# Kernel tuning notes

Hardware: AMD Instinct MI355X
Metric: run time of the kernel (lower is better)

The kernel has to match this reference:

```python
import jax, jax.numpy as jnp
import numpy as np

DIM = 96
HEADS = 4
HID = int(DIM * 2.66)  # 255, GDFN hidden width
B, H, W = 4, 128, 128


def _conv(x, w, b=None, groups=1):
    y = jax.lax.conv_general_dilated(x, w, (1, 1), 'SAME',
                                     dimension_numbers=('NCHW', 'OIHW', 'NCHW'),
                                     feature_group_count=groups)
    return y if b is None else y + b[None, :, None, None]


def _ln(x, w, b):
    # WithBias LayerNorm over channel dim (per pixel), biased variance, eps=1e-5
    mu = x.mean(1, keepdims=True)
    var = ((x - mu) ** 2).mean(1, keepdims=True)
    return (x - mu) / jnp.sqrt(var + 1e-5) * w[None, :, None, None] + b[None, :, None, None]


def _l2norm(x):
    # torch F.normalize(dim=-1): x / max(||x||_2, 1e-12)
    return x / jnp.maximum(jnp.linalg.norm(x, axis=-1, keepdims=True), 1e-12)


def _gelu(x):
    return jax.nn.gelu(x, approximate=False)


def setup_inputs() -> dict:
    key = jax.random.key(0)
    ks = iter(jax.random.split(key, 32))
    nrm = lambda shp, s=0.02: jax.random.normal(next(ks), shp, dtype=jnp.float32) * s
    d, h2 = DIM, HID
    inp = {
        'x': jax.random.normal(next(ks), (B, DIM, H, W), dtype=jnp.float32),
        # L_conv: 3x3(d->d,+b) GELU 1x1(d->1,+b)
        'Lc_w1': nrm((d, d, 3, 3)), 'Lc_b1': jnp.zeros((d,), jnp.float32),
        'Lc_w2': nrm((1, d, 1, 1)), 'Lc_b2': jnp.zeros((1,), jnp.float32),
        # R_conv: 3x3(d->d,+b) GELU 1x1(d->3,+b)
        'Rc_w1': nrm((d, d, 3, 3)), 'Rc_b1': jnp.zeros((d,), jnp.float32),
        'Rc_w2': nrm((3, d, 1, 1)), 'Rc_b2': jnp.zeros((3,), jnp.float32),
        # L_rein: 3x3(1->d,+b) GELU ; R_rein: 3x3(3->d,+b)
        'Lr_w': nrm((d, 1, 3, 3)), 'Lr_b': jnp.zeros((d,), jnp.float32),
        'Rr_w': nrm((d, 3, 3, 3)), 'Rr_b': jnp.zeros((d,), jnp.float32),
        # LayerNorms (WithBias)
        'n1_w': jnp.ones((d,), jnp.float32), 'n1_b': jnp.zeros((d,), jnp.float32),
        'nL_w': jnp.ones((d,), jnp.float32), 'nL_b': jnp.zeros((d,), jnp.float32),
        'n2_w': jnp.ones((d,), jnp.float32), 'n2_b': jnp.zeros((d,), jnp.float32),
        # Illum_Attention (bias=False)
        'temp': jnp.ones((HEADS, 1, 1), jnp.float32),
        'q_w': nrm((d, d, 1, 1)),
        'qd_w': nrm((d, d, 3, 3)),          # q_dwconv is a FULL 3x3 conv (no groups)
        'kv_w': nrm((2 * d, d, 1, 1)),
        'kvd_w': nrm((2 * d, 1, 3, 3)),     # depthwise, groups=2*dim
        'po_w': nrm((d, d, 1, 1)),
        # FeedForward (bias=False); NOTE: 'dwconv' here is a FULL 3x3 conv
        'pi_w': nrm((h2, d, 1, 1)),
        'fdw_w': nrm((h2, h2, 3, 3)),
        'fpo_w': nrm((d, h2, 1, 1)),
    }
    return inp


def reference(x, Lc_w1, Lc_b1, Lc_w2, Lc_b2, Rc_w1, Rc_b1, Rc_w2, Rc_b2,
              Lr_w, Lr_b, Rr_w, Rr_b, n1_w, n1_b, nL_w, nL_b, n2_w, n2_b,
              temp, q_w, qd_w, kv_w, kvd_w, po_w, pi_w, fdw_w, fpo_w):
    b, c, h, w = x.shape
    # Retinex decomposition heads
    L = _conv(_gelu(_conv(x, Lc_w1, Lc_b1)), Lc_w2, Lc_b2)   # [b,1,h,w]
    R = _conv(_gelu(_conv(x, Rc_w1, Rc_b1)), Rc_w2, Rc_b2)   # [b,3,h,w]
    L_rein = _gelu(_conv(jax.lax.stop_gradient(L), Lr_w, Lr_b))  # detach in torch
    R_rein = _conv(jax.lax.stop_gradient(R), Rr_w, Rr_b)
    # Illum_Guided_TransformerBlock: x = x + attn(norm1(x), normL(illum))
    xn = _ln(x, n1_w, n1_b)
    ill = _ln(L_rein, nL_w, nL_b)
    q = _conv(_conv(ill, q_w), qd_w)
    kv = _conv(_conv(xn, kv_w), kvd_w, groups=2 * c)
    k, v = jnp.split(kv, 2, axis=1)
    ch, hw = c // HEADS, h * w
    heads = lambda t: t.reshape(b, HEADS, ch, hw)
    qh, kh, vh = _l2norm(heads(q)), _l2norm(heads(k)), heads(v)
    # channel-wise attention: [b,heads,ch,ch]
    attn = jax.nn.softmax(jnp.einsum('bhci,bhdi->bhcd', qh, kh) * temp[None], axis=-1)
    out = jnp.einsum('bhcd,bhdi->bhci', attn, vh).reshape(b, c, h, w)
    x = x + _conv(out, po_w)
    # x = x + ffn(norm2(x))
    x2 = _ln(x, n2_w, n2_b)
    x = x + _conv(_gelu(_conv(_conv(x2, pi_w), fdw_w)), fpo_w)
    x = x + R_rein
    return (x, L, R)
```

## Files before the change

### kernel.cpp

```cpp
#include <hip/hip_runtime.h>

#define HWsz 16384
#define Wd 128

typedef unsigned short ushortT;
typedef unsigned int uintT;
typedef __attribute__((ext_vector_type(8))) short short8v;
typedef __attribute__((ext_vector_type(4))) float f32x4;
typedef __attribute__((ext_vector_type(16))) float f32x16;
typedef __attribute__((ext_vector_type(4))) unsigned short ushort4v;

__device__ __forceinline__ float gelu_f(float x){
    return 0.5f * x * (1.0f + erff(x * 0.70710678118654752f));
}
__device__ __forceinline__ ushortT f2b(float f){
    union { float f; uintT u; } v; v.f = f;
    uintT r = v.u + 0x7FFFu + ((v.u >> 16) & 1u);
    return (ushortT)(r >> 16);
}
__device__ __forceinline__ float b2f(ushortT u){
    union { uintT u; float f; } v; v.u = ((uintT)u) << 16; return v.f;
}
__device__ __forceinline__ void gload_lds16(const ushortT* g, ushortT* l){
    __builtin_amdgcn_global_load_lds(
        (const __attribute__((address_space(1))) void*)g,
        (__attribute__((address_space(3))) void*)l, 16, 0, 0);
}

__device__ __forceinline__ void pack3_one(int e, const float* __restrict__ w,
    ushortT* __restrict__ outp, int cout, int cin, int BN, int NCH)
{
    int j = e & 7; int r = e >> 3;
    int ocl = r % BN; r /= BN;
    int kg  = r & 3;  r >>= 2;
    int tap = r % 9;  r /= 9;
    int ch  = r % NCH;
    int nt  = r / NCH;
    int ci = ch*32 + kg*8 + j;
    int oc = nt*BN + ocl;
    float v = (oc < cout && ci < cin) ? w[((size_t)oc*cin + ci)*9 + tap] : 0.f;
    outp[e] = f2b(v);
}
__device__ __forceinline__ void pack1_one(int e, const float* __restrict__ w,
    ushortT* __restrict__ outp, int cout, int cin, int BN, int NCH)
{
    int j = e & 7; int r = e >> 3;
    int ocl = r % BN; r /= BN;
    int kg  = r & 3;  r >>= 2;
    int ch  = r % NCH;
    int nt  = r / NCH;
    int ci = ch*32 + kg*8 + j;
    int oc = nt*BN + ocl;
    float v = (oc < cout && ci < cin) ? w[(size_t)oc*cin + ci] : 0.f;
    outp[e] = f2b(v);
}
__global__ __launch_bounds__(256) void pack_all_kernel(
    const float* Lc, const float* Rc, const float* Qd, const float* Fd,
    const float* Q1, const float* KV1, const float* PI1, const float* FPO1,
    ushortT* dL, ushortT* dR, ushortT* dQ, ushortT* dF,
    ushortT* dq0, ushortT* dkv, ushortT* dpi, ushortT* dfpo)
{
    int e = blockIdx.x*256 + threadIdx.x;
    if      (e < 82944)  pack3_one(e,        Lc, dL, 96, 96, 48, 3);
    else if (e < 165888) pack3_one(e-82944,  Rc, dR, 96, 96, 48, 3);
    else if (e < 248832) pack3_one(e-165888, Qd, dQ, 96, 96, 32, 3);
    else if (e < 912384) pack3_one(e-248832, Fd, dF, 255,255, 48, 8);
    else if (e < 921600) pack1_one(e-912384, Q1, dq0, 96, 96, 96, 3);
    else if (e < 940032) pack1_one(e-921600, KV1,dkv, 192,96, 48, 3);
    else if (e < 964608) pack1_one(e-940032, PI1,dpi, 255,96, 64, 3);
    else if (e < 989184) pack1_one(e-964608, FPO1,dfpo,96,255, 96, 8);
}

__global__ __launch_bounds__(256) void tonhwc_ln_kernel(
    const float* __restrict__ in, const float* __restrict__ w,
    const float* __restrict__ bias, ushortT* __restrict__ xh,
    ushortT* __restrict__ xnh)
{
    const int p = blockIdx.x*256 + threadIdx.x;
    const int b = blockIdx.y;
    const float* ip = in + (size_t)b*96*HWsz + p;
    float v[96]; float s=0.f;
#pragma unroll
    for(int c=0;c<96;c++){ v[c]=ip[(size_t)c*HWsz]; s+=v[c]; }
    const float mu = s*(1.f/96.f);
    float s2=0.f;
#pragma unroll
    for(int c=0;c<96;c++){ float d=v[c]-mu; s2+=d*d; }
    const float inv = 1.f/sqrtf(s2*(1.f/96.f)+1e-5f);
    ushortT* op1 = xh  + ((size_t)b*HWsz + p)*96;
    ushortT* op2 = xnh + ((size_t)b*HWsz + p)*96;
#pragma unroll
    for (int g=0; g<12; g++){
        uint4 pk1, pk2; uintT a4[4], n4[4];
#pragma unroll
        for (int i=0;i<4;i++){
            float x0 = v[g*8+2*i], x1v = v[g*8+2*i+1];
            a4[i] = (uintT)f2b(x0) | ((uintT)f2b(x1v)<<16);
            float r0 = (x0-mu)*inv*w[g*8+2*i]+bias[g*8+2*i];
            float r1 = (x1v-mu)*inv*w[g*8+2*i+1]+bias[g*8+2*i+1];
            n4[i] = (uintT)f2b(r0) | ((uintT)f2b(r1)<<16);
        }
        pk1.x=a4[0]; pk1.y=a4[1]; pk1.z=a4[2]; pk1.w=a4[3];
        pk2.x=n4[0]; pk2.y=n4[1]; pk2.z=n4[2]; pk2.w=n4[3];
        *(uint4*)(op1 + g*8) = pk1;
        *(uint4*)(op2 + g*8) = pk2;
    }
}

template<int NG, int NCH, int ACT, int TWOOUT>
__global__ __launch_bounds__(256,3) void conv3x3_v4(
    const ushortT* __restrict__ inh,
    const ushortT* __restrict__ wpk1, const ushortT* __restrict__ wpk2,
    const float* __restrict__ bias1, const float* __restrict__ bias2,
    ushortT* __restrict__ out1, ushortT* __restrict__ out2,
    int cout, int ocpad)
{
    constexpr int BN = NG*16;
    constexpr int Cpad = NCH*32;
    constexpr int WCH4 = 9*4*BN;
    constexpr int WI = (WCH4 + 255)/256;
    __shared__ __align__(16) ushortT As[4*324*8];
    __shared__ __align__(16) ushortT Ws[WCH4*8];

    const int tid = threadIdx.x;
    const int l   = tid & 63;
    const int wv  = tid >> 6;
    const int l15 = l & 15;
    const int kg  = l >> 4;
    const int tix = blockIdx.x & 7, tiy = blockIdx.x >> 3;
    const int b   = blockIdx.z;
    const int x0 = tix*16, y0 = tiy*16;

    int nt = blockIdx.y;
    const ushortT* wpk; const float* bias; ushortT* outp; int ntw;
    if (TWOOUT && nt >= 2){ wpk = wpk2; bias = bias2; outp = out2; ntw = nt-2; }
    else { wpk = wpk1; bias = bias1; outp = out1; ntw = nt; }
    const int ocbase = ntw*BN;

    f32x4 acc[4][NG];
#pragma unroll
    for (int m=0;m<4;m++)
#pragma unroll
        for (int n=0;n<NG;n++) acc[m][n] = (f32x4){0.f,0.f,0.f,0.f};

    const ushortT* inb = inh + (size_t)b*HWsz*Cpad;

    for (int ch=0; ch<NCH; ch++){
        __syncthreads();
        for (int t=tid; t<1296; t+=256){
            int p = t>>2, g = t&3;
            int hy = p/18, hx = p - hy*18;
            int gy = y0 + hy - 1, gx = x0 + hx - 1;
            uint4 v; v.x=0u; v.y=0u; v.z=0u; v.w=0u;
            if ((unsigned)gy < 128u && (unsigned)gx < 128u)
                v = *(const uint4*)(inb + (size_t)(gy*Wd+gx)*Cpad + ch*32 + g*8);
            *(uint4*)(As + (g*324+p)*8) = v;
        }
        {
            const ushortT* wsrc = wpk + ((size_t)ntw*NCH + ch)*(WCH4*8);
#pragma unroll
            for (int i=0; i<WI; i++){
                int t = i*256 + tid;
                if ((WCH4 & 255) == 0 || t < WCH4)
                    gload_lds16(wsrc + (size_t)t*8, Ws + (size_t)t*8);
            }
        }
        __syncthreads();
#pragma unroll
        for (int tp=0; tp<9; tp++){
            const int dy = tp/3, dx = tp - dy*3;
            short8v bf[NG];
#pragma unroll
            for (int n=0;n<NG;n++)
                bf[n] = *(const short8v*)(Ws + ((size_t)(tp*4 + kg)*BN + n*16 + l15)*8);
#pragma unroll
            for (int mg=0;mg<4;mg++){
                short8v a = *(const short8v*)(As + (kg*324 + (wv*4+mg+dy)*18 + l15+dx)*8);
#pragma unroll
                for (int n=0;n<NG;n++)
                    acc[mg][n] = __builtin_amdgcn_mfma_f32_16x16x32_bf16(a, bf[n], acc[mg][n], 0,0,0);
            }
        }
    }
    __syncthreads();
    ushortT* Ts = As + wv*1024;
#pragma unroll
    for (int mg=0;mg<4;mg++){
        int gy = y0 + wv*4 + mg;
        ushortT* orow = outp + ((size_t)b*HWsz + gy*Wd + x0)*ocpad + ocbase;
#pragma unroll
        for (int n=0;n<NG;n++){
            int ocl = n*16 + l15;
            int oc  = ocbase + ocl;
            float bs = (bias && oc < cout) ? bias[oc] : 0.f;
#pragma unroll
            for (int j=0;j<4;j++){
                int pxj = kg*4 + j;
                float r = 0.f;
                if (oc < cout){ r = acc[mg][n][j] + bs; if (ACT) r = gelu_f(r); }
                int seg = ((ocl>>3) + pxj) & 7;
                Ts[pxj*64 + seg*8 + (ocl&7)] = f2b(r);
            }
        }
#pragma unroll
        for (int ps=0; ps < (BN+31)/32; ps++){
            int rpx = l & 15;
            int rs  = (l>>4) + ps*4;
            if (rs*8 < BN){
                int pseg = (rs + rpx) & 7;
                short8v v = *(const short8v*)(Ts + rpx*64 + pseg*8);
                *(short8v*)(orow + (size_t)rpx*ocpad + rs*8) = v;
            }
        }
    }
}

template<int NGW, int NCH>
__global__ __launch_bounds__(256) void gemm1x1_v2(
    const ushortT* __restrict__ inh, const ushortT* __restrict__ wpk,
    ushortT* __restrict__ outp, int cout, int ocpad)
{
    constexpr int BN = NGW*16;
    constexpr int Cpad = NCH*32;
    __shared__ __align__(16) ushortT Ts[4*16*64];

    const int tid = threadIdx.x;
    const int l = tid & 63, wv = tid >> 6, l15 = l & 15, kg = l >> 4;
    const int p0 = blockIdx.x*64;
    const int b  = blockIdx.z;
    const int nt = wv, ocbase = wv*BN;
    const ushortT* inb = inh + (size_t)b*HWsz*Cpad;

    f32x4 acc[4][NGW];
#pragma unroll
    for (int m=0;m<4;m++)
#pragma unroll
        for (int n=0;n<NGW;n++) acc[m][n] = (f32x4){0.f,0.f,0.f,0.f};

#pragma unroll
    for (int ch=0; ch<NCH; ch++){
        short8v a[4], bw[NGW];
#pragma unroll
        for (int mg=0; mg<4; mg++)
            a[mg] = *(const short8v*)(inb + (size_t)(p0 + mg*16 + l15)*Cpad + ch*32 + kg*8);
#pragma unroll
        for (int n=0;n<NGW;n++)
            bw[n] = *(const short8v*)(wpk + (((size_t)(nt*NCH + ch)*4 + kg)*BN + n*16 + l15)*8);
#pragma unroll
        for (int mg=0;mg<4;mg++)
#pragma unroll
            for (int n=0;n<NGW;n++)
                acc[mg][n] = __builtin_amdgcn_mfma_f32_16x16x32_bf16(a[mg], bw[n], acc[mg][n], 0,0,0);
    }
    ushortT* Tw = Ts + wv*1024;
#pragma unroll
    for (int mg=0;mg<4;mg++){
        ushortT* orow = outp + ((size_t)b*HWsz + p0 + mg*16)*ocpad + ocbase;
#pragma unroll
        for (int n=0;n<NGW;n++){
            int ocl = n*16 + l15;
            int oc  = ocbase + ocl;
#pragma unroll
            for (int j=0;j<4;j++){
                int pxj = kg*4 + j;
                float r = (oc < cout) ? acc[mg][n][j] : 0.f;
                int seg = ((ocl>>3) + pxj) & 7;
                Tw[pxj*64 + seg*8 + (ocl&7)] = f2b(r);
            }
        }
#pragma unroll
        for (int ps=0; ps < (BN+31)/32; ps++){
            int rpx = l & 15;
            int rs  = (l>>4) + ps*4;
            if (rs*8 < BN){
                int pseg = (rs + rpx) & 7;
                short8v v = *(const short8v*)(Tw + rpx*64 + pseg*8);
                *(short8v*)(orow + (size_t)rpx*ocpad + rs*8) = v;
            }
        }
    }
}

template<int NG, int NCH, int ACT, int OMODE, int NSPLIT, int XMAP>
__global__ __launch_bounds__(256,4) void conv3x3_mfma(
    const ushortT* __restrict__ inh,
    const ushortT* __restrict__ wpk1, const ushortT* __restrict__ wpk2,
    const float* __restrict__ bias1, const float* __restrict__ bias2,
    void* __restrict__ out1, void* __restrict__ out2,
    int cout, int ocpad)
{
    constexpr int BN = NG*16;
    constexpr int Cpad = NCH*32;
    __shared__ __align__(16) ushortT As[4*324*8];

    const int tid = threadIdx.x;
    const int l   = tid & 63;
    const int wv  = tid >> 6;
    const int l15 = l & 15;
    const int kg  = l >> 4;
    int tile = blockIdx.x, nt = blockIdx.y, b = blockIdx.z;
    const int tix = tile & 7, tiy = tile >> 3;

    const ushortT* wpk = wpk1; const float* bias = bias1; void* outv = out1;
    if (NSPLIT > 0 && nt >= NSPLIT){ nt -= NSPLIT; wpk = wpk2; bias = bias2; outv = out2; }

    f32x4 acc[4][NG];
#pragma unroll
    for (int m=0;m<4;m++)
#pragma unroll
        for (int n=0;n<NG;n++) acc[m][n] = (f32x4){0.f,0.f,0.f,0.f};

    const ushortT* inb = inh + (size_t)b*HWsz*Cpad;

    for (int ch=0; ch<NCH; ch++){
        __syncthreads();
#pragma unroll
        for (int g=0; g<4; g++){
            for (int p=tid; p<324; p+=256){
                int hy = p/18, hx = p - hy*18;
                int gy = tiy*16 + hy - 1, gx = tix*16 + hx - 1;
                uint4 v; v.x=0u; v.y=0u; v.z=0u; v.w=0u;
                if ((unsigned)gy < 128u && (unsigned)gx < 128u)
                    v = *(const uint4*)(inb + (size_t)(gy*Wd+gx)*Cpad + ch*32 + g*8);
                *(uint4*)(As + (g*324+p)*8) = v;
            }
        }
        __syncthreads();
        const ushortT* wch = wpk + (size_t)(nt*NCH + ch)*(9*4*BN*8);
#pragma unroll
        for (int tp=0; tp<9; tp++){
            const int dy = tp/3, dx = tp - dy*3;
            short8v a[4], bf[NG];
#pragma unroll
            for (int mg=0; mg<4; mg++){
                int p = (wv*4 + mg + dy)*18 + l15 + dx;
                a[mg] = *(const short8v*)(As + (kg*324 + p)*8);
            }
#pragma unroll
            for (int n=0;n<NG;n++)
                bf[n] = *(const short8v*)(wch + ((size_t)(tp*4 + kg)*BN + n*16 + l15)*8);
#pragma unroll
            for (int mg=0;mg<4;mg++)
#pragma unroll
                for (int n=0;n<NG;n++)
                    acc[mg][n] = __builtin_amdgcn_mfma_f32_16x16x32_bf16(a[mg], bf[n], acc[mg][n], 0,0,0);
        }
    }
    if (OMODE == 2){
        ushortT* out = (ushortT*)outv;
#pragma unroll
        for (int n=0;n<NG;n++){
            int oc = nt*BN + n*16 + l15;
            if (oc < cout){
                float bs = bias ? bias[oc] : 0.f;
#pragma unroll
                for (int mg=0;mg<4;mg++){
                    int gy = tiy*16 + wv*4 + mg;
                    int gx = tix*16 + kg*4;
                    ushort4v pk;
#pragma unroll
                    for (int j=0;j<4;j++){
                        float r = acc[mg][n][j] + bs;
                        if (ACT) r = gelu_f(r);
                        pk[j] = f2b(r);
                    }
                    *(ushort4v*)(out + ((size_t)b*cout + oc)*HWsz + gy*Wd + gx) = pk;
                }
            }
        }
    }
}

template<int NG, int NCH, int RES, int OMODE, int XMAP>
__global__ __launch_bounds__(256) void gemm1x1_mfma(
    const ushortT* __restrict__ inh, const ushortT* __restrict__ wpk, int wstride_z,
    const float* __restrict__ res1, const ushortT* __restrict__ res2b,
    void* __restrict__ outv, int cout, int ocpad)
{
    constexpr int BN = NG*16;
    constexpr int Cpad = NCH*32;
    constexpr int LSTR = (BN <= 64) ? 64 : 128;
    constexpr int MASK = LSTR/8 - 1;
    __shared__ __align__(16) ushortT TsS[(OMODE==1) ? 4*16*LSTR : 16];

    const int tid = threadIdx.x;
    const int l = tid & 63, wv = tid >> 6, l15 = l & 15, kg = l >> 4;
    int chunk = blockIdx.x, nt = blockIdx.y, b = blockIdx.z;
    const int p0 = chunk*256 + wv*64;
    const ushortT* inb = inh + (size_t)b*HWsz*Cpad;
    const ushortT* wp  = wpk + (size_t)b*wstride_z;

    f32x4 acc[4][NG];
#pragma unroll
    for (int m=0;m<4;m++)
#pragma unroll
        for (int n=0;n<NG;n++) acc[m][n] = (f32x4){0.f,0.f,0.f,0.f};

#pragma unroll
    for (int ch=0; ch<NCH; ch++){
        short8v a[4], bw[NG];
#pragma unroll
        for (int mg=0; mg<4; mg++)
            a[mg] = *(const short8v*)(inb + (size_t)(p0 + mg*16 + l15)*Cpad + ch*32 + kg*8);
#pragma unroll
        for (int n=0;n<NG;n++)
            bw[n] = *(const short8v*)(wp + (((size_t)(nt*NCH + ch)*4 + kg)*BN + n*16 + l15)*8);
#pragma unroll
        for (int mg=0;mg<4;mg++)
#pragma unroll
            for (int n=0;n<NG;n++)
                acc[mg][n] = __builtin_amdgcn_mfma_f32_16x16x32_bf16(a[mg], bw[n], acc[mg][n], 0,0,0);
    }
    if (OMODE == 0){
        float* out = (float*)outv;
#pragma unroll
        for (int n=0;n<NG;n++){
            int oc = nt*BN + n*16 + l15;
            if (oc < cout){
#pragma unroll
                for (int mg=0;mg<4;mg++){
                    int pix = p0 + mg*16 + kg*4;
                    size_t idx = ((size_t)b*cout + oc)*HWsz + pix;
                    float4 r;
                    r.x = acc[mg][n][0]; r.y = acc[mg][n][1];
                    r.z = acc[mg][n][2]; r.w = acc[mg][n][3];
                    if (RES>=1){ float4 q = *(const float4*)(res1+idx); r.x+=q.x;r.y+=q.y;r.z+=q.z;r.w+=q.w; }
                    if (RES>=2){
                        ushort4v q = *(const ushort4v*)(res2b+idx);
                        r.x+=b2f(q[0]); r.y+=b2f(q[1]); r.z+=b2f(q[2]); r.w+=b2f(q[3]);
                    }
                    *(float4*)(out + idx) = r;
                }
            }
        }
    } else {
        ushortT* outp = (ushortT*)outv;
        ushortT* Ts = TsS + wv*(16*LSTR);
#pragma unroll
        for (int mg=0;mg<4;mg++){
            ushortT* orow = outp + ((size_t)b*HWsz + p0 + mg*16)*ocpad + nt*BN;
#pragma unroll
            for (int n=0;n<NG;n++){
                int ocl = n*16 + l15;
                int oc  = nt*BN + ocl;
#pragma unroll
                for (int j=0;j<4;j++){
                    int pxj = kg*4 + j;
                    float r = (oc < cout) ? acc[mg][n][j] : 0.f;
                    int seg = ((ocl>>3) + pxj) & MASK;
                    Ts[pxj*LSTR + seg*8 + (ocl&7)] = f2b(r);
                }
            }
#pragma unroll
            for (int ps=0; ps < (BN+31)/32; ps++){
                int rpx = l & 15;
                int rs  = (l>>4) + ps*4;
                if (rs*8 < BN){
                    int pseg = (rs + rpx) & MASK;
                    short8v v = *(const short8v*)(Ts + rpx*LSTR + pseg*8);
                    *(short8v*)(orow + (size_t)rpx*ocpad + rs*8) = v;
                }
            }
        }
    }
}

__global__ __launch_bounds__(256) void pvpo_ln_kernel(
    const ushortT* __restrict__ vh, const ushortT* __restrict__ Mpk,
    const float* __restrict__ xres, const float* __restrict__ lnw,
    const float* __restrict__ lnb, float* __restrict__ x1out,
    ushortT* __restrict__ x2nh)
{
    constexpr int BN = 96, NG = 6, NCH = 3, Cpad = 96, LSTR = 128, MASK = 15;
    __shared__ __align__(16) ushortT TsS[4*16*LSTR];

    const int tid = threadIdx.x;
    const int l = tid & 63, wv = tid >> 6, l15 = l & 15, kg = l >> 4;
    const int b = blockIdx.z;
    const int p0 = blockIdx.x*256 + wv*64;
    const ushortT* inb = vh + (size_t)b*HWsz*Cpad;
    const ushortT* wp  = Mpk + (size_t)b*9216;

    f32x4 acc[4][NG];
#pragma unroll
    for (int m=0;m<4;m++)
#pragma unroll
        for (int n=0;n<NG;n++) acc[m][n] = (f32x4){0.f,0.f,0.f,0.f};

#pragma unroll
    for (int ch=0; ch<NCH; ch++){
        short8v a[4], bw[NG];
#pragma unroll
        for (int mg=0; mg<4; mg++)
            a[mg] = *(const short8v*)(inb + (size_t)(p0 + mg*16 + l15)*Cpad + ch*32 + kg*8);
#pragma unroll
        for (int n=0;n<NG;n++)
            bw[n] = *(const short8v*)(wp + (((size_t)ch*4 + kg)*BN + n*16 + l15)*8);
#pragma unroll
        for (int mg=0;mg<4;mg++)
#pragma unroll
            for (int n=0;n<NG;n++)
                acc[mg][n] = __builtin_amdgcn_mfma_f32_16x16x32_bf16(a[mg], bw[n], acc[mg][n], 0,0,0);
    }
    float mu_[4], inv_[4];
#pragma unroll
    for (int mg=0;mg<4;mg++){
#pragma unroll
        for (int n=0;n<NG;n++){
            int oc = n*16 + l15;
            int pix = p0 + mg*16 + kg*4;
            size_t idx = ((size_t)b*96 + oc)*HWsz + pix;
            float4 q = *(const float4*)(xres+idx);
            acc[mg][n][0] += q.x; acc[mg][n][1] += q.y;
            acc[mg][n][2] += q.z; acc[mg][n][3] += q.w;
            float4 r;
            r.x = acc[mg][n][0]; r.y = acc[mg][n][1];
            r.z = acc[mg][n][2]; r.w = acc[mg][n][3];
            *(float4*)(x1out + idx) = r;
        }
    }
    float nv[4][NG][4];
#pragma unroll
    for (int mg=0;mg<4;mg++){
#pragma unroll
        for (int j=0;j<4;j++){
            float s = 0.f, s2 = 0.f;
#pragma unroll
            for (int n=0;n<NG;n++){ float v = acc[mg][n][j]; s += v; s2 += v*v; }
#pragma unroll
            for (int m=1; m<16; m<<=1){
                s  += __shfl_xor(s, m, 64);
                s2 += __shfl_xor(s2, m, 64);
            }
            float mu = s*(1.f/96.f);
            float var = s2*(1.f/96.f) - mu*mu;
            float inv = 1.f/sqrtf(var + 1e-5f);
#pragma unroll
            for (int n=0;n<NG;n++){
                int oc = n*16 + l15;
                nv[mg][n][j] = (acc[mg][n][j]-mu)*inv*lnw[oc]+lnb[oc];
            }
        }
    }
    ushortT* Ts = TsS + wv*(16*LSTR);
#pragma unroll
    for (int mg=0;mg<4;mg++){
        ushortT* orow = x2nh + ((size_t)b*HWsz + p0 + mg*16)*96;
#pragma unroll
        for (int n=0;n<NG;n++){
            int ocl = n*16 + l15;
#pragma unroll
            for (int j=0;j<4;j++){
                int pxj = kg*4 + j;
                int seg = ((ocl>>3) + pxj) & MASK;
                Ts[pxj*LSTR + seg*8 + (ocl&7)] = f2b(nv[mg][n][j]);
            }
        }
#pragma unroll
        for (int ps=0; ps<3; ps++){
            int rpx = l & 15;
            int rs  = (l>>4) + ps*4;
            int pseg = (rs + rpx) & MASK;
            short8v v = *(const short8v*)(Ts + rpx*LSTR + pseg*8);
            *(short8v*)(orow + (size_t)rpx*96 + rs*8) = v;
        }
    }
}

template<int NOUT>
__global__ __launch_bounds__(256) void head1x1_kernel(
    const ushortT* __restrict__ inh, const float* __restrict__ w,
    const float* __restrict__ bias, float* __restrict__ out)
{
    __shared__ float lw[NOUT*96];
    const int tid = threadIdx.x;
    for (int t=tid; t<NOUT*96; t+=256) lw[t] = w[t];
    __syncthreads();
    const int p = blockIdx.x*256 + tid;
    const int b = blockIdx.y;
    const ushortT* ip = inh + ((size_t)b*HWsz + p)*96;
    float v[96];
#pragma unroll
    for (int g=0; g<12; g++){
        short8v s = *(const short8v*)(ip + g*8);
#pragma unroll
        for (int i=0;i<8;i++) v[g*8+i] = b2f((ushortT)s[i]);
    }
#pragma unroll
    for (int oc=0; oc<NOUT; oc++){
        float acc = bias[oc];
#pragma unroll
        for (int c=0;c<96;c++) acc += v[c]*lw[oc*96+c];
        out[((size_t)b*NOUT + oc)*HWsz + p] = acc;
    }
}

__global__ __launch_bounds__(256) void lrein_ln_kernel(
    const float* __restrict__ L, const float* __restrict__ w,
    const float* __restrict__ bias, const float* __restrict__ lnw,
    const float* __restrict__ lnb, ushortT* __restrict__ outh)
{
    __shared__ float sw[864], sb[96], sn1[96], sn2[96];
    const int tid = threadIdx.x;
    for (int t=tid; t<864; t+=256) sw[t] = w[t];
    if (tid < 96){ sb[tid]=bias[tid]; sn1[tid]=lnw[tid]; sn2[tid]=lnb[tid]; }
    __syncthreads();
    const int p = blockIdx.x*256 + tid;
    const int b = blockIdx.y;
    const int y = p>>7, x = p&127;
    const float* ib = L + (size_t)b*HWsz;
    float win[9];
#pragma unroll
    for (int dy=0;dy<3;dy++)
#pragma unroll
        for (int dx=0;dx<3;dx++){
            int gy=y+dy-1, gx=x+dx-1;
            win[dy*3+dx] = ((unsigned)gy<128u && (unsigned)gx<128u) ? ib[gy*Wd+gx] : 0.f;
        }
    float v[96]; float s=0.f;
#pragma unroll
    for (int c=0;c<96;c++){
        float a = sb[c];
#pragma unroll
        for (int t=0;t<9;t++) a += win[t]*sw[c*9+t];
        a = gelu_f(a);
        v[c]=a; s+=a;
    }
    const float mu = s*(1.f/96.f);
    float s2=0.f;
#pragma unroll
    for (int c=0;c<96;c++){ float d=v[c]-mu; s2+=d*d; }
    const float inv = 1.f/sqrtf(s2*(1.f/96.f)+1e-5f);
    ushortT* op = outh + ((size_t)b*HWsz + p)*96;
#pragma unroll
    for (int g=0; g<12; g++){
        uint4 pk; uintT w4[4];
#pragma unroll
        for (int i=0;i<4;i++){
            float r0 = (v[g*8+2*i]-mu)*inv*sn1[g*8+2*i]+sn2[g*8+2*i];
            float r1 = (v[g*8+2*i+1]-mu)*inv*sn1[g*8+2*i+1]+sn2[g*8+2*i+1];
            w4[i] = (uintT)f2b(r0) | ((uintT)f2b(r1)<<16);
        }
        pk.x=w4[0]; pk.y=w4[1]; pk.z=w4[2]; pk.w=w4[3];
        *(uint4*)(op + g*8) = pk;
    }
}

__global__ __launch_bounds__(256) void conv3x3_rr_kernel(
    const float* __restrict__ in, const float* __restrict__ w,
    const float* __restrict__ bias, ushortT* __restrict__ out)
{
    __shared__ float sw[216], sb[8];
    const int oc0 = blockIdx.y*8;
    if (threadIdx.x < 216) sw[threadIdx.x] = w[(size_t)oc0*27 + threadIdx.x];
    if (threadIdx.x < 8)   sb[threadIdx.x] = bias[oc0 + threadIdx.x];
    __syncthreads();
    const int p = blockIdx.x*256+threadIdx.x;
    const int b = blockIdx.z;
    const int y=p>>7, x=p&127;
    const float* ib = in + (size_t)b*3*HWsz;
    float win[27];
#pragma unroll
    for (int ci=0;ci<3;ci++)
#pragma unroll
        for (int dy=0;dy<3;dy++)
#pragma unroll
            for (int dx=0;dx<3;dx++){
                int gy=y+dy-1, gx=x+dx-1;
                win[ci*9+dy*3+dx] = ((unsigned)gy<128u && (unsigned)gx<128u)
                    ? ib[(size_t)ci*HWsz + gy*Wd+gx] : 0.f;
            }
#pragma unroll
    for (int i=0;i<8;i++){
        float acc = sb[i];
#pragma unroll
        for (int t=0;t<27;t++) acc += win[t]*sw[i*27+t];
        out[((size_t)b*96 + oc0+i)*HWsz + p] = f2b(acc);
    }
}

__global__ __launch_bounds__(256) void dw_nhwc_kernel(
    const ushortT* __restrict__ inh, const float* __restrict__ w,
    ushortT* __restrict__ kout, ushortT* __restrict__ vouth)
{
    const int p = blockIdx.x*256+threadIdx.x;
    const int c0 = blockIdx.y*8;
    const int b = blockIdx.z;
    const int y=p>>7, x=p&127;
    float lw[72];
#pragma unroll
    for (int i=0;i<8;i++)
#pragma unroll
        for (int t=0;t<9;t++) lw[i*9+t] = w[(size_t)(c0+i)*9 + t];
    const ushortT* ib = inh + (size_t)b*HWsz*192;
    float acc[8];
#pragma unroll
    for (int i=0;i<8;i++) acc[i]=0.f;
#pragma unroll
    for(int dy=0;dy<3;dy++){
        int gy=y+dy-1;
        if((unsigned)gy<128u){
#pragma unroll
            for(int dx=0;dx<3;dx++){
                int gx=x+dx-1;
                if((unsigned)gx<128u){
                    short8v s = *(const short8v*)(ib + (size_t)(gy*Wd+gx)*192 + c0);
#pragma unroll
                    for (int i=0;i<8;i++) acc[i] += b2f((ushortT)s[i])*lw[i*9+dy*3+dx];
                }
            }
        }
    }
    if (c0 < 96){
#pragma unroll
        for (int i=0;i<8;i++)
            kout[((size_t)b*96 + c0+i)*HWsz + p] = f2b(acc[i]);
    } else {
        ushortT* op = vouth + ((size_t)b*HWsz + p)*96 + (c0-96);
        uint4 pk;
        pk.x = (uintT)f2b(acc[0]) | ((uintT)f2b(acc[1])<<16);
        pk.y = (uintT)f2b(acc[2]) | ((uintT)f2b(acc[3])<<16);
        pk.z = (uintT)f2b(acc[4]) | ((uintT)f2b(acc[5])<<16);
        pk.w = (uintT)f2b(acc[6]) | ((uintT)f2b(acc[7])<<16);
        *(uint4*)op = pk;
    }
}

__global__ __launch_bounds__(256) void rownorm_bf16_kernel(
    const ushortT* __restrict__ qb, const ushortT* __restrict__ kb,
    float* __restrict__ invqk)
{
    __shared__ float red[256];
    const int r = blockIdx.x;
    const ushortT* ip = (r < 384) ? (qb + (size_t)r*HWsz) : (kb + (size_t)(r-384)*HWsz);
    float s=0.f;
    const ushortT* tp = ip + threadIdx.x*64;
#pragma unroll
    for (int g=0; g<8; g++){
        short8v v = *(const short8v*)(tp + g*8);
#pragma unroll
        for (int i=0;i<8;i++){ float f = b2f((ushortT)v[i]); s += f*f; }
    }
    red[threadIdx.x]=s; __syncthreads();
    for(int st=128; st>0; st>>=1){
        if(threadIdx.x<st) red[threadIdx.x]+=red[threadIdx.x+st];
        __syncthreads();
    }
    if(threadIdx.x==0) invqk[r] = 1.f/fmaxf(sqrtf(red[0]), 1e-12f);
}

__global__ __launch_bounds__(256) void qk_mfma_kernel(
    const ushortT* __restrict__ qb, const ushortT* __restrict__ kb,
    float* __restrict__ part)
{
    const int tid = threadIdx.x;
    const int l = tid & 63, wv = tid >> 6;
    const int chunk = blockIdx.x*4 + wv;
    const int bh = blockIdx.y, b = bh>>2, h = bh&3;
    const int ch = min(l & 31, 23);
    const int kh = (l >> 5)*8;
    const ushortT* qp = qb + ((size_t)b*96 + h*24 + ch)*HWsz + chunk*512 + kh;
    const ushortT* kp = kb + ((size_t)b*96 + h*24 + ch)*HWsz + chunk*512 + kh;
    f32x16 acc;
#pragma unroll
    for (int r=0;r<16;r++) acc[r]=0.f;
    for (int ks=0; ks<32; ks++){
        short8v a  = *(const short8v*)(qp + ks*16);
        short8v bb = *(const short8v*)(kp + ks*16);
        acc = __builtin_amdgcn_mfma_f32_32x32x16_bf16(a, bb, acc, 0,0,0);
    }
    float* op = part + ((size_t)chunk*16 + bh)*1024;
    const int col = l & 31;
#pragma unroll
    for (int r=0;r<16;r++){
        int row = (r&3) + 8*(r>>2) + 4*(l>>5);
        op[row*32 + col] = acc[r];
    }
}

__global__ void qk_reduce_kernel(const float* __restrict__ part, float* __restrict__ out)
{
    int idx = blockIdx.x*256+threadIdx.x;
    float s=0.f;
    for(int c=0;c<32;c++) s += part[(size_t)c*16384 + idx];
    out[idx]=s;
}

__global__ __launch_bounds__(576) void softmax_kernel(
    const float* __restrict__ raw, const float* __restrict__ invq,
    const float* __restrict__ invk, const float* __restrict__ temp,
    float* __restrict__ attn)
{
    __shared__ float l[576];
    const int bh=blockIdx.x, b=bh>>2, h=bh&3;
    const int tid=threadIdx.x;
    const int i=tid/24, j=tid-i*24;
    l[tid] = raw[(size_t)bh*1024 + i*32 + j] * invq[b*96+h*24+i] * invk[b*96+h*24+j] * temp[h];
    __syncthreads();
    if(tid<24){
        float m=-1e30f;
#pragma unroll
        for(int jj=0;jj<24;jj++) m = fmaxf(m, l[tid*24+jj]);
        float e[24]; float s=0.f;
#pragma unroll
        for(int jj=0;jj<24;jj++){ e[jj]=__expf(l[tid*24+jj]-m); s+=e[jj]; }
        float isv = 1.f/s;
#pragma unroll
        for(int jj=0;jj<24;jj++) attn[(size_t)bh*576 + tid*24 + jj] = e[jj]*isv;
    }
}

__global__ __launch_bounds__(256) void mkM_kernel(
    const float* __restrict__ attn, const float* __restrict__ po_w,
    ushortT* __restrict__ Mpk)
{
    const int b = blockIdx.x;
    for (int e = threadIdx.x; e < 9216; e += 256){
        int oc = e / 96, d = e - oc*96;
        int h = d / 24, dl = d - h*24;
        const float* aw = attn + ((size_t)(b*4+h))*576 + dl;
        const float* pw = po_w + (size_t)oc*96 + h*24;
        float s = 0.f;
#pragma unroll
        for (int c=0;c<24;c++) s += pw[c]*aw[c*24];
        int ch = d>>5, kg = (d>>3)&3, j = d&7;
        Mpk[(size_t)b*9216 + ((size_t)(ch*4+kg)*96 + oc)*8 + j] = f2b(s);
    }
}

extern "C" void kernel_launch(void* const* d_in, const int* in_sizes, int n_in,
                              void* d_out, int out_size, void* d_ws, size_t ws_size,
                              hipStream_t stream)
{
    const float* x     = (const float*)d_in[0];
    const float* Lc_w1 = (const float*)d_in[1];
    const float* Lc_b1 = (const float*)d_in[2];
    const float* Lc_w2 = (const float*)d_in[3];
    const float* Lc_b2 = (const float*)d_in[4];
    const float* Rc_w1 = (const float*)d_in[5];
    const float* Rc_b1 = (const float*)d_in[6];
    const float* Rc_w2 = (const float*)d_in[7];
    const float* Rc_b2 = (const float*)d_in[8];
    const float* Lr_w  = (const float*)d_in[9];
    const float* Lr_b  = (const float*)d_in[10];
    const float* Rr_w  = (const float*)d_in[11];
    const float* Rr_b  = (const float*)d_in[12];
    const float* n1_w  = (const float*)d_in[13];
    const float* n1_b  = (const float*)d_in[14];
    const float* nL_w  = (const float*)d_in[15];
    const float* nL_b  = (const float*)d_in[16];
    const float* n2_w  = (const float*)d_in[17];
    const float* n2_b  = (const float*)d_in[18];
    const float* temp  = (const float*)d_in[19];
    const float* q_w   = (const float*)d_in[20];
    const float* qd_w  = (const float*)d_in[21];
    const float* kv_w  = (const float*)d_in[22];
    const float* kvd_w = (const float*)d_in[23];
    const float* po_w  = (const float*)d_in[24];
    const float* pi_w  = (const float*)d_in[25];
    const float* fdw_w = (const float*)d_in[26];
    const float* fpo_w = (const float*)d_in[27];

    char* base = (char*)d_ws;
    ushortT* xh   = (ushortT*)(base + 0);
    ushortT* f0h  = (ushortT*)(base + 0);
    ushortT* Lh   = (ushortT*)(base + 33554432);
    ushortT* kv0h = (ushortT*)(base + 33554432);
    ushortT* f1h  = (ushortT*)(base + 33554432);
    ushortT* Rh   = (ushortT*)(base + 67108864);
    ushortT* vh   = (ushortT*)(base + 67108864);
    ushortT* x2nh = (ushortT*)(base + 67108864);
    ushortT* illh = (ushortT*)(base + 79691776);
    ushortT* xnh  = (ushortT*)(base + 92274688);
    ushortT* q0h  = (ushortT*)(base + 104857600);
    ushortT* qb   = (ushortT*)(base + 117440512);
    float*   x1   = (float*)(base + 117440512);
    ushortT* kb   = (ushortT*)(base + 142606336);
    ushortT* Bb   = (ushortT*)(base + 155189248);
    char* smb = base + 167772160;
    ushortT* wpkL = (ushortT*)smb;   smb += 165888;
    ushortT* wpkR = (ushortT*)smb;   smb += 165888;
    ushortT* wpkQ = (ushortT*)smb;   smb += 165888;
    ushortT* wpkF = (ushortT*)smb;   smb += 1327104;
    ushortT* wq0  = (ushortT*)smb;   smb += 18432;
    ushortT* wkv  = (ushortT*)smb;   smb += 36864;
    ushortT* wpi  = (ushortT*)smb;   smb += 49152;
    ushortT* wfpo = (ushortT*)smb;   smb += 49152;
    ushortT* Mpk  = (ushortT*)smb;   smb += 73728;
    float* invqk  = (float*)smb;     smb += 3072;
    float* part   = (float*)smb;     smb += 2097152;
    float* araw   = (float*)smb;     smb += 65536;
    float* attn   = (float*)smb;     smb += 36864;

    float* out_x = (float*)d_out;
    float* out_L = out_x + (size_t)4*96*HWsz;
    float* out_R = out_L + (size_t)4*HWsz;

    dim3 blk(256);

    hipLaunchKernelGGL(pack_all_kernel, dim3(3864), blk, 0, stream,
        Lc_w1, Rc_w1, qd_w, fdw_w, q_w, kv_w, pi_w, fpo_w,
        wpkL, wpkR, wpkQ, wpkF, wq0, wkv, wpi, wfpo);
    hipLaunchKernelGGL(tonhwc_ln_kernel, dim3(64,4), blk, 0, stream, x, n1_w, n1_b, xh, xnh);

    hipLaunchKernelGGL((conv3x3_v4<3,3,1,1>), dim3(64,4,4), blk, 0, stream,
        xh, wpkL, wpkR, Lc_b1, Rc_b1, Lh, Rh, 96, 96);
    hipLaunchKernelGGL((head1x1_kernel<1>), dim3(64,4), blk, 0, stream, Lh, Lc_w2, Lc_b2, out_L);
    hipLaunchKernelGGL((head1x1_kernel<3>), dim3(64,4), blk, 0, stream, Rh, Rc_w2, Rc_b2, out_R);
    hipLaunchKernelGGL(lrein_ln_kernel, dim3(64,4), blk, 0, stream, out_L, Lr_w, Lr_b, nL_w, nL_b, illh);
    hipLaunchKernelGGL(conv3x3_rr_kernel, dim3(64,12,4), blk, 0, stream, out_R, Rr_w, Rr_b, Bb);

    hipLaunchKernelGGL((gemm1x1_mfma<6,3,0,1,0>), dim3(64,1,4), blk, 0, stream,
        illh, wq0, 0, nullptr, nullptr, (void*)q0h, 96, 96);
    hipLaunchKernelGGL((conv3x3_mfma<2,3,0,2,0,0>), dim3(64,3,4), blk, 0, stream,
        q0h, wpkQ, wpkQ, nullptr, nullptr, (void*)qb, (void*)qb, 96, 0);
    hipLaunchKernelGGL((gemm1x1_v2<3,3>), dim3(256,1,4), blk, 0, stream,
        xnh, wkv, kv0h, 192, 192);
    hipLaunchKernelGGL(dw_nhwc_kernel, dim3(64,24,4), blk, 0, stream, kv0h, kvd_w, kb, vh);

    hipLaunchKernelGGL(rownorm_bf16_kernel, dim3(768), blk, 0, stream, qb, kb, invqk);
    hipLaunchKernelGGL(qk_mfma_kernel, dim3(8,16), blk, 0, stream, qb, kb, part);
    hipLaunchKernelGGL(qk_reduce_kernel, dim3(64), blk, 0, stream, part, araw);
    hipLaunchKernelGGL(softmax_kernel, dim3(16), dim3(576), 0, stream, araw, invqk, invqk+384, temp, attn);
    hipLaunchKernelGGL(mkM_kernel, dim3(4), blk, 0, stream, attn, po_w, Mpk);
    hipLaunchKernelGGL(pvpo_ln_kernel, dim3(64,1,4), blk, 0, stream,
        vh, Mpk, x, n2_w, n2_b, x1, x2nh);

    hipLaunchKernelGGL((gemm1x1_v2<4,3>), dim3(256,1,4), blk, 0, stream,
        x2nh, wpi, f0h, 255, 256);
    hipLaunchKernelGGL((conv3x3_v4<3,8,1,0>), dim3(64,6,4), blk, 0, stream,
        f0h, wpkF, wpkF, nullptr, nullptr, f1h, f1h, 255, 256);
    hipLaunchKernelGGL((gemm1x1_mfma<6,8,2,0,0>), dim3(64,1,4), blk, 0, stream,
        f1h, wfpo, 0, x1, Bb, (void*)out_x, 96, 0);
}
```

Before: 373.6 us.

## Add two-batch 3x3 conv tiles, reuse v4 conv for q, fuse qk reduce into softmax

Adds conv3x3_tt, which processes two batch images per block so each weight chunk loaded into LDS is reused across both images. The Lc/Rc and FFN depthwise-replacement 3x3 convs now use it, with half as many blocks. The q 3x3 conv switches to conv3x3_v4 with a new planar output mode and a 48-wide N tile. The qk partial reduction is folded into the softmax kernel, and LN variance becomes two-pass. Changes touch occupancy (launch bounds 2, doubled LDS) and remove one launch.

```diff
diff --git a/kernel.cpp b/kernel.cpp
--- a/kernel.cpp
+++ b/kernel.cpp
@@ -63,7 +63,7 @@
     int e = blockIdx.x*256 + threadIdx.x;
     if      (e < 82944)  pack3_one(e,        Lc, dL, 96, 96, 48, 3);
     else if (e < 165888) pack3_one(e-82944,  Rc, dR, 96, 96, 48, 3);
-    else if (e < 248832) pack3_one(e-165888, Qd, dQ, 96, 96, 32, 3);
+    else if (e < 248832) pack3_one(e-165888, Qd, dQ, 96, 96, 48, 3);
     else if (e < 912384) pack3_one(e-248832, Fd, dF, 255,255, 48, 8);
     else if (e < 921600) pack1_one(e-912384, Q1, dq0, 96, 96, 96, 3);
     else if (e < 940032) pack1_one(e-921600, KV1,dkv, 192,96, 48, 3);
@@ -108,6 +108,125 @@
 }
 
 template<int NG, int NCH, int ACT, int TWOOUT>
+__global__ __launch_bounds__(256,2) void conv3x3_tt(
+    const ushortT* __restrict__ inh,
+    const ushortT* __restrict__ wpk1, const ushortT* __restrict__ wpk2,
+    const float* __restrict__ bias1, const float* __restrict__ bias2,
+    ushortT* __restrict__ out1, ushortT* __restrict__ out2,
+    int cout, int ocpad)
+{
+    constexpr int BN = NG*16;
+    constexpr int Cpad = NCH*32;
+    constexpr int WCH4 = 9*4*BN;
+    constexpr int WI = (WCH4 + 255)/256;
+    __shared__ __align__(16) ushortT As[2*4*324*8];
+    __shared__ __align__(16) ushortT Ws[WCH4*8];
+
+    const int tid = threadIdx.x;
+    const int l   = tid & 63;
+    const int wv  = tid >> 6;
+    const int l15 = l & 15;
+    const int kg  = l >> 4;
+    const int tix = blockIdx.x & 7, tiy = blockIdx.x >> 3;
+    const int b0  = blockIdx.z*2;
+    const int x0 = tix*16, y0 = tiy*16;
+
+    int nt = blockIdx.y;
+    const ushortT* wpk; const float* bias; ushortT* outp; int ntw;
+    if (TWOOUT && nt >= 2){ wpk = wpk2; bias = bias2; outp = out2; ntw = nt-2; }
+    else { wpk = wpk1; bias = bias1; outp = out1; ntw = nt; }
+    const int ocbase = ntw*BN;
+
+    f32x4 acc[2][4][NG];
+#pragma unroll
+    for (int tl=0;tl<2;tl++)
+#pragma unroll
+        for (int m=0;m<4;m++)
+#pragma unroll
+            for (int n=0;n<NG;n++) acc[tl][m][n] = (f32x4){0.f,0.f,0.f,0.f};
+
+    for (int ch=0; ch<NCH; ch++){
+        __syncthreads();
+#pragma unroll
+        for (int tl=0; tl<2; tl++){
+            const ushortT* inb = inh + (size_t)(b0+tl)*HWsz*Cpad;
+            for (int t=tid; t<1296; t+=256){
+                int p = t>>2, g = t&3;
+                int hy = p/18, hx = p - hy*18;
+                int gy = y0 + hy - 1, gx = x0 + hx - 1;
+                uint4 v; v.x=0u; v.y=0u; v.z=0u; v.w=0u;
+                if ((unsigned)gy < 128u && (unsigned)gx < 128u)
+                    v = *(const uint4*)(inb + (size_t)(gy*Wd+gx)*Cpad + ch*32 + g*8);
+                *(uint4*)(As + (tl*1296 + g*324 + p)*8) = v;
+            }
+        }
+        {
+            const ushortT* wsrc = wpk + ((size_t)ntw*NCH + ch)*(WCH4*8);
+#pragma unroll
+            for (int i=0; i<WI; i++){
+                int t = i*256 + tid;
+                if ((WCH4 & 255) == 0 || t < WCH4)
+                    gload_lds16(wsrc + (size_t)t*8, Ws + (size_t)t*8);
+            }
+        }
+        __syncthreads();
+#pragma unroll
+        for (int tp=0; tp<9; tp++){
+            const int dy = tp/3, dx = tp - dy*3;
+            short8v bf[NG];
+#pragma unroll
+            for (int n=0;n<NG;n++)
+                bf[n] = *(const short8v*)(Ws + ((size_t)(tp*4 + kg)*BN + n*16 + l15)*8);
+#pragma unroll
+            for (int tl=0;tl<2;tl++){
+#pragma unroll
+                for (int mg=0;mg<4;mg++){
+                    short8v a = *(const short8v*)(As + (tl*1296 + kg*324 + (wv*4+mg+dy)*18 + l15+dx)*8);
+#pragma unroll
+                    for (int n=0;n<NG;n++)
+                        acc[tl][mg][n] = __builtin_amdgcn_mfma_f32_16x16x32_bf16(a, bf[n], acc[tl][mg][n], 0,0,0);
+                }
+            }
+        }
+    }
+    __syncthreads();
+    ushortT* Ts = As + wv*1024;
+#pragma unroll
+    for (int tl=0;tl<2;tl++){
+        ushortT* outb = outp + (size_t)(b0+tl)*HWsz*ocpad;
+#pragma unroll
+        for (int mg=0;mg<4;mg++){
+            int gy = y0 + wv*4 + mg;
+            ushortT* orow = outb + ((size_t)gy*Wd + x0)*ocpad + ocbase;
+#pragma unroll
+            for (int n=0;n<NG;n++){
+                int ocl = n*16 + l15;
+                int oc  = ocbase + ocl;
+                float bs = (bias && oc < cout) ? bias[oc] : 0.f;
+#pragma unroll
+                for (int j=0;j<4;j++){
+                    int pxj = kg*4 + j;
+                    float r = 0.f;
+                    if (oc < cout){ r = acc[tl][mg][n][j] + bs; if (ACT) r = gelu_f(r); }
+                    int seg = ((ocl>>3) + pxj) & 7;
+                    Ts[pxj*64 + seg*8 + (ocl&7)] = f2b(r);
+                }
+            }
+#pragma unroll
+            for (int ps=0; ps < (BN+31)/32; ps++){
+                int rpx = l & 15;
+                int rs  = (l>>4) + ps*4;
+                if (rs*8 < BN && ocbase + rs*8 + 8 <= ocpad){
+                    int pseg = (rs + rpx) & 7;
+                    short8v v = *(const short8v*)(Ts + rpx*64 + pseg*8);
+                    *(short8v*)(orow + (size_t)rpx*ocpad + rs*8) = v;
+                }
+            }
+        }
+    }
+}
+
+template<int NG, int NCH, int ACT, int TWOOUT, int OMODE>
 __global__ __launch_bounds__(256,3) void conv3x3_v4(
     const ushortT* __restrict__ inh,
     const ushortT* __restrict__ wpk1, const ushortT* __restrict__ wpk2,
@@ -182,34 +301,57 @@
             }
         }
     }
-    __syncthreads();
-    ushortT* Ts = As + wv*1024;
-#pragma unroll
-    for (int mg=0;mg<4;mg++){
-        int gy = y0 + wv*4 + mg;
-        ushortT* orow = outp + ((size_t)b*HWsz + gy*Wd + x0)*ocpad + ocbase;
+    if (OMODE == 1){
+        __syncthreads();
+        ushortT* Ts = As + wv*1024;
+#pragma unroll
+        for (int mg=0;mg<4;mg++){
+            int gy = y0 + wv*4 + mg;
+            ushortT* orow = outp + ((size_t)b*HWsz + gy*Wd + x0)*ocpad + ocbase;
+#pragma unroll
+            for (int n=0;n<NG;n++){
+                int ocl = n*16 + l15;
+                int oc  = ocbase + ocl;
+                float bs = (bias && oc < cout) ? bias[oc] : 0.f;
+#pragma unroll
+                for (int j=0;j<4;j++){
+                    int pxj = kg*4 + j;
+                    float r = 0.f;
+                    if (oc < cout){ r = acc[mg][n][j] + bs; if (ACT) r = gelu_f(r); }
+                    int seg = ((ocl>>3) + pxj) & 7;
+                    Ts[pxj*64 + seg*8 + (ocl&7)] = f2b(r);
+                }
+            }
+#pragma unroll
+            for (int ps=0; ps < (BN+31)/32; ps++){
+                int rpx = l & 15;
+                int rs  = (l>>4) + ps*4;
+                if (rs*8 < BN && ocbase + rs*8 + 8 <= ocpad){
+                    int pseg = (rs + rpx) & 7;
+                    short8v v = *(const short8v*)(Ts + rpx*64 + pseg*8);
+                    *(short8v*)(orow + (size_t)rpx*ocpad + rs*8) = v;
+                }
+            }
+        }
+    } else {
 #pragma unroll
         for (int n=0;n<NG;n++){
-            int ocl = n*16 + l15;
-            int oc  = ocbase + ocl;
-            float bs = (bias && oc < cout) ? bias[oc] : 0.f;
-#pragma unroll
-            for (int j=0;j<4;j++){
-                int pxj = kg*4 + j;
-                float r = 0.f;
-                if (oc < cout){ r = acc[mg][n][j] + bs; if (ACT) r = gelu_f(r); }
-                int seg = ((ocl>>3) + pxj) & 7;
-                Ts[pxj*64 + seg*8 + (ocl&7)] = f2b(r);
-            }
-        }
-#pragma unroll
-        for (int ps=0; ps < (BN+31)/32; ps++){
-            int rpx = l & 15;
-            int rs  = (l>>4) + ps*4;
-            if (rs*8 < BN){
-                int pseg = (rs + rpx) & 7;
-                short8v v = *(const short8v*)(Ts + rpx*64 + pseg*8);
-                *(short8v*)(orow + (size_t)rpx*ocpad + rs*8) = v;
+            int oc = ocbase + n*16 + l15;
+            if (oc < cout){
+                float bs = bias ? bias[oc] : 0.f;
+#pragma unroll
+                for (int mg=0;mg<4;mg++){
+                    int gy = y0 + wv*4 + mg;
+                    int gx = x0 + kg*4;
+                    ushort4v pk;
+#pragma unroll
+                    for (int j=0;j<4;j++){
+                        float r = acc[mg][n][j] + bs;
+                        if (ACT) r = gelu_f(r);
+                        pk[j] = f2b(r);
+                    }
+                    *(ushort4v*)(outp + ((size_t)b*cout + oc)*HWsz + gy*Wd + gx) = pk;
+                }
             }
         }
     }
@@ -276,96 +418,6 @@
                 int pseg = (rs + rpx) & 7;
                 short8v v = *(const short8v*)(Tw + rpx*64 + pseg*8);
                 *(short8v*)(orow + (size_t)rpx*ocpad + rs*8) = v;
-            }
-        }
-    }
-}
-
-template<int NG, int NCH, int ACT, int OMODE, int NSPLIT, int XMAP>
-__global__ __launch_bounds__(256,4) void conv3x3_mfma(
-    const ushortT* __restrict__ inh,
-    const ushortT* __restrict__ wpk1, const ushortT* __restrict__ wpk2,
-    const float* __restrict__ bias1, const float* __restrict__ bias2,
-    void* __restrict__ out1, void* __restrict__ out2,
-    int cout, int ocpad)
-{
-    constexpr int BN = NG*16;
-    constexpr int Cpad = NCH*32;
-    __shared__ __align__(16) ushortT As[4*324*8];
-
-    const int tid = threadIdx.x;
-    const int l   = tid & 63;
-    const int wv  = tid >> 6;
-    const int l15 = l & 15;
-    const int kg  = l >> 4;
-    int tile = blockIdx.x, nt = blockIdx.y, b = blockIdx.z;
-    const int tix = tile & 7, tiy = tile >> 3;
-
-    const ushortT* wpk = wpk1; const float* bias = bias1; void* outv = out1;
-    if (NSPLIT > 0 && nt >= NSPLIT){ nt -= NSPLIT; wpk = wpk2; bias = bias2; outv = out2; }
-
-    f32x4 acc[4][NG];
-#pragma unroll
-    for (int m=0;m<4;m++)
-#pragma unroll
-        for (int n=0;n<NG;n++) acc[m][n] = (f32x4){0.f,0.f,0.f,0.f};
-
-    const ushortT* inb = inh + (size_t)b*HWsz*Cpad;
-
-    for (int ch=0; ch<NCH; ch++){
-        __syncthreads();
-#pragma unroll
-        for (int g=0; g<4; g++){
-            for (int p=tid; p<324; p+=256){
-                int hy = p/18, hx = p - hy*18;
-                int gy = tiy*16 + hy - 1, gx = tix*16 + hx - 1;
-                uint4 v; v.x=0u; v.y=0u; v.z=0u; v.w=0u;
-                if ((unsigned)gy < 128u && (unsigned)gx < 128u)
-                    v = *(const uint4*)(inb + (size_t)(gy*Wd+gx)*Cpad + ch*32 + g*8);
-                *(uint4*)(As + (g*324+p)*8) = v;
-            }
-        }
-        __syncthreads();
-        const ushortT* wch = wpk + (size_t)(nt*NCH + ch)*(9*4*BN*8);
-#pragma unroll
-        for (int tp=0; tp<9; tp++){
-            const int dy = tp/3, dx = tp - dy*3;
-            short8v a[4], bf[NG];
-#pragma unroll
-            for (int mg=0; mg<4; mg++){
-                int p = (wv*4 + mg + dy)*18 + l15 + dx;
-                a[mg] = *(const short8v*)(As + (kg*324 + p)*8);
-            }
-#pragma unroll
-            for (int n=0;n<NG;n++)
-                bf[n] = *(const short8v*)(wch + ((size_t)(tp*4 + kg)*BN + n*16 + l15)*8);
-#pragma unroll
-            for (int mg=0;mg<4;mg++)
-#pragma unroll
-                for (int n=0;n<NG;n++)
-                    acc[mg][n] = __builtin_amdgcn_mfma_f32_16x16x32_bf16(a[mg], bf[n], acc[mg][n], 0,0,0);
-        }
-    }
-    if (OMODE == 2){
-        ushortT* out = (ushortT*)outv;
-#pragma unroll
-        for (int n=0;n<NG;n++){
-            int oc = nt*BN + n*16 + l15;
-            if (oc < cout){
-                float bs = bias ? bias[oc] : 0.f;
-#pragma unroll
-                for (int mg=0;mg<4;mg++){
-                    int gy = tiy*16 + wv*4 + mg;
-                    int gx = tix*16 + kg*4;
-                    ushort4v pk;
-#pragma unroll
-                    for (int j=0;j<4;j++){
-                        float r = acc[mg][n][j] + bs;
-                        if (ACT) r = gelu_f(r);
-                        pk[j] = f2b(r);
-                    }
-                    *(ushort4v*)(out + ((size_t)b*cout + oc)*HWsz + gy*Wd + gx) = pk;
-                }
             }
         }
     }
@@ -502,7 +554,6 @@
             for (int n=0;n<NG;n++)
                 acc[mg][n] = __builtin_amdgcn_mfma_f32_16x16x32_bf16(a[mg], bw[n], acc[mg][n], 0,0,0);
     }
-    float mu_[4], inv_[4];
 #pragma unroll
     for (int mg=0;mg<4;mg++){
 #pragma unroll
@@ -524,17 +575,18 @@
     for (int mg=0;mg<4;mg++){
 #pragma unroll
         for (int j=0;j<4;j++){
-            float s = 0.f, s2 = 0.f;
-#pragma unroll
-            for (int n=0;n<NG;n++){ float v = acc[mg][n][j]; s += v; s2 += v*v; }
-#pragma unroll
-            for (int m=1; m<16; m<<=1){
-                s  += __shfl_xor(s, m, 64);
-                s2 += __shfl_xor(s2, m, 64);
-            }
+            float s = 0.f;
+#pragma unroll
+            for (int n=0;n<NG;n++) s += acc[mg][n][j];
+#pragma unroll
+            for (int m=1; m<16; m<<=1) s += __shfl_xor(s, m, 64);
             float mu = s*(1.f/96.f);
-            float var = s2*(1.f/96.f) - mu*mu;
-            float inv = 1.f/sqrtf(var + 1e-5f);
+            float s2 = 0.f;
+#pragma unroll
+            for (int n=0;n<NG;n++){ float d = acc[mg][n][j]-mu; s2 += d*d; }
+#pragma unroll
+            for (int m=1; m<16; m<<=1) s2 += __shfl_xor(s2, m, 64);
+            float inv = 1.f/sqrtf(s2*(1.f/96.f) + 1e-5f);
 #pragma unroll
             for (int n=0;n<NG;n++){
                 int oc = n*16 + l15;
@@ -778,16 +830,8 @@
     }
 }
 
-__global__ void qk_reduce_kernel(const float* __restrict__ part, float* __restrict__ out)
-{
-    int idx = blockIdx.x*256+threadIdx.x;
-    float s=0.f;
-    for(int c=0;c<32;c++) s += part[(size_t)c*16384 + idx];
-    out[idx]=s;
-}
-
 __global__ __launch_bounds__(576) void softmax_kernel(
-    const float* __restrict__ raw, const float* __restrict__ invq,
+    const float* __restrict__ part, const float* __restrict__ invq,
     const float* __restrict__ invk, const float* __restrict__ temp,
     float* __restrict__ attn)
 {
@@ -795,16 +839,18 @@
     const int bh=blockIdx.x, b=bh>>2, h=bh&3;
     const int tid=threadIdx.x;
     const int i=tid/24, j=tid-i*24;
-    l[tid] = raw[(size_t)bh*1024 + i*32 + j] * invq[b*96+h*24+i] * invk[b*96+h*24+j] * temp[h];
+    float s=0.f;
+    for (int c=0;c<32;c++) s += part[((size_t)c*16 + bh)*1024 + i*32 + j];
+    l[tid] = s * invq[b*96+h*24+i] * invk[b*96+h*24+j] * temp[h];
     __syncthreads();
     if(tid<24){
         float m=-1e30f;
 #pragma unroll
         for(int jj=0;jj<24;jj++) m = fmaxf(m, l[tid*24+jj]);
-        float e[24]; float s=0.f;
-#pragma unroll
-        for(int jj=0;jj<24;jj++){ e[jj]=__expf(l[tid*24+jj]-m); s+=e[jj]; }
-        float isv = 1.f/s;
+        float e[24]; float sm=0.f;
+#pragma unroll
+        for(int jj=0;jj<24;jj++){ e[jj]=__expf(l[tid*24+jj]-m); sm+=e[jj]; }
+        float isv = 1.f/sm;
 #pragma unroll
         for(int jj=0;jj<24;jj++) attn[(size_t)bh*576 + tid*24 + jj] = e[jj]*isv;
     }
@@ -889,7 +935,6 @@
     ushortT* Mpk  = (ushortT*)smb;   smb += 73728;
     float* invqk  = (float*)smb;     smb += 3072;
     float* part   = (float*)smb;     smb += 2097152;
-    float* araw   = (float*)smb;     smb += 65536;
     float* attn   = (float*)smb;     smb += 36864;
 
     float* out_x = (float*)d_out;
@@ -903,7 +948,7 @@
         wpkL, wpkR, wpkQ, wpkF, wq0, wkv, wpi, wfpo);
     hipLaunchKernelGGL(tonhwc_ln_kernel, dim3(64,4), blk, 0, stream, x, n1_w, n1_b, xh, xnh);
 
-    hipLaunchKernelGGL((conv3x3_v4<3,3,1,1>), dim3(64,4,4), blk, 0, stream,
+    hipLaunchKernelGGL((conv3x3_tt<3,3,1,1>), dim3(64,4,2), blk, 0, stream,
         xh, wpkL, wpkR, Lc_b1, Rc_b1, Lh, Rh, 96, 96);
     hipLaunchKernelGGL((head1x1_kernel<1>), dim3(64,4), blk, 0, stream, Lh, Lc_w2, Lc_b2, out_L);
     hipLaunchKernelGGL((head1x1_kernel<3>), dim3(64,4), blk, 0, stream, Rh, Rc_w2, Rc_b2, out_R);
@@ -912,23 +957,22 @@
 
     hipLaunchKernelGGL((gemm1x1_mfma<6,3,0,1,0>), dim3(64,1,4), blk, 0, stream,
         illh, wq0, 0, nullptr, nullptr, (void*)q0h, 96, 96);
-    hipLaunchKernelGGL((conv3x3_mfma<2,3,0,2,0,0>), dim3(64,3,4), blk, 0, stream,
-        q0h, wpkQ, wpkQ, nullptr, nullptr, (void*)qb, (void*)qb, 96, 0);
+    hipLaunchKernelGGL((conv3x3_v4<3,3,0,0,2>), dim3(64,2,4), blk, 0, stream,
+        q0h, wpkQ, wpkQ, nullptr, nullptr, qb, qb, 96, 0);
     hipLaunchKernelGGL((gemm1x1_v2<3,3>), dim3(256,1,4), blk, 0, stream,
         xnh, wkv, kv0h, 192, 192);
     hipLaunchKernelGGL(dw_nhwc_kernel, dim3(64,24,4), blk, 0, stream, kv0h, kvd_w, kb, vh);
 
     hipLaunchKernelGGL(rownorm_bf16_kernel, dim3(768), blk, 0, stream, qb, kb, invqk);
     hipLaunchKernelGGL(qk_mfma_kernel, dim3(8,16), blk, 0, stream, qb, kb, part);
-    hipLaunchKernelGGL(qk_reduce_kernel, dim3(64), blk, 0, stream, part, araw);
-    hipLaunchKernelGGL(softmax_kernel, dim3(16), dim3(576), 0, stream, araw, invqk, invqk+384, temp, attn);
+    hipLaunchKernelGGL(softmax_kernel, dim3(16), dim3(576), 0, stream, part, invqk, invqk+384, temp, attn);
     hipLaunchKernelGGL(mkM_kernel, dim3(4), blk, 0, stream, attn, po_w, Mpk);
     hipLaunchKernelGGL(pvpo_ln_kernel, dim3(64,1,4), blk, 0, stream,
         vh, Mpk, x, n2_w, n2_b, x1, x2nh);
 
     hipLaunchKernelGGL((gemm1x1_v2<4,3>), dim3(256,1,4), blk, 0, stream,
         x2nh, wpi, f0h, 255, 256);
-    hipLaunchKernelGGL((conv3x3_v4<3,8,1,0>), dim3(64,6,4), blk, 0, stream,
+    hipLaunchKernelGGL((conv3x3_tt<3,8,1,0>), dim3(64,6,2), blk, 0, stream,
         f0h, wpkF, wpkF, nullptr, nullptr, f1h, f1h, 255, 256);
     hipLaunchKernelGGL((gemm1x1_mfma<6,8,2,0,0>), dim3(64,1,4), blk, 0, stream,
         f1h, wfpo, 0, x1, Bb, (void*)out_x, 96, 0);
```

New measurement: 460.3 us. +23.2%, slower.
